# Performance work log

Measured on AMD Instinct MI355X. Metric: run time of the kernel, lower is better.

The kernel has to match this reference:

```python
import jax, jax.numpy as jnp
import numpy as np

DIM = 768
NC = 8            # ncontext
SIGMA = 0.5       # mask_sigma
SCALE = DIM ** (-0.5)
B, N = 256, 205   # N = 1 (CLS) + 14*14 (patches) + NC (concept tokens)


def setup_inputs() -> dict:
    key = jax.random.key(0)
    k1, k2, k3, k4 = jax.random.split(key, 4)
    x = jax.random.normal(k1, (B, N, DIM), dtype=jnp.float32)
    s = DIM ** (-0.5)
    Wq = jax.random.normal(k2, (DIM, DIM), dtype=jnp.float32) * s
    Wk = jax.random.normal(k3, (DIM, DIM), dtype=jnp.float32) * s
    Wv = jax.random.normal(k4, (DIM, DIM), dtype=jnp.float32) * s
    return {"x": x, "Wq": Wq, "Wk": Wk, "Wv": Wv}


def mask_attention_map(region):
    # region: [B, NC, HW] raw attention scores over the patch grid
    Bc, C, HW = region.shape
    H = W = int(np.sqrt(HW))  # 14
    amap = region.reshape(Bc, C, H, W)
    loc = jnp.argmax(amap.reshape(Bc, C, -1), axis=2)  # flat argmax (non-differentiable)
    max_y = (loc // H).astype(jnp.float32)[:, :, None, None]  # row of max
    max_x = (loc % H).astype(jnp.float32)[:, :, None, None]   # col of max
    # Faithful to torch.meshgrid(x, y) 'ij' + reshape(H, W): xx varies along rows,
    # yy varies along cols, and xx is compared to max_x (col), yy to max_y (row).
    rows = jnp.arange(H, dtype=jnp.float32).reshape(1, 1, H, 1)  # xx
    cols = jnp.arange(W, dtype=jnp.float32).reshape(1, 1, 1, W)  # yy
    g = jnp.exp(-((rows - max_x) ** 2 + (cols - max_y) ** 2) / (2.0 * SIGMA ** 2))
    g = g / jnp.max(g.reshape(Bc, C, -1), axis=2)[:, :, None, None]
    return (amap * g).reshape(Bc, C, HW)


def reference(x, Wq, Wk, Wv):
    # nn.Linear(dim, dim, bias=False): y = x @ W.T
    q = jnp.einsum('bnd,ed->bne', x, Wq)
    k = jnp.einsum('bnd,ed->bne', x, Wk)
    v = jnp.einsum('bnd,ed->bne', x, Wv)
    attn = jnp.einsum('bqd,bkd->bqk', q, k)  # [B, N, N] raw scores
    # gaussian-mask the concept-token -> patch region (pre-softmax, in-place write-back)
    region = mask_attention_map(attn[:, -NC:, 1:-NC])
    attn = attn.at[:, -NC:, 1:-NC].set(region)
    attn = jax.nn.softmax(attn * SCALE, axis=-1)
    out = jnp.einsum('bqk,bkd->bqd', attn, v)
    return attn[:, None], out
```

## Files before the change

### kernel.cpp

```cpp
#include <hip/hip_runtime.h>
#include <hip/hip_bf16.h>

#define NB   256
#define NT   205
#define DIMD 768
#define NCC  8
#define NPP  196
#define LDY  1536
#define SCL  0.03608439182435161f

using u16 = unsigned short;
using u32 = unsigned int;
using bf16x8 = __attribute__((ext_vector_type(8))) short;
using f32x4  = __attribute__((ext_vector_type(4))) float;

#define WS_WB   0ul
#define WS_YV   3538944ul
#define WS_PB   164757504ul
#define DO_OUT  43033600ul
#define DO_XB   43033600ul
#define DO_M    143696896ul
#define DO_Z    149988352ul
#define DO_REGM 157885440ul

__device__ __forceinline__ u16 f2bf(float f) {
  u32 u = __float_as_uint(f);
  u += 0x7FFFu + ((u >> 16) & 1u);
  return (u16)(u >> 16);
}

__device__ __forceinline__ void gld16(const void* g, void* l) {
  __builtin_amdgcn_global_load_lds((const __attribute__((address_space(1))) u32*)g,
                                   (__attribute__((address_space(3))) u32*)l, 16, 0, 0);
}

__device__ __forceinline__ f32x4 mfma16(bf16x8 a, bf16x8 b, f32x4 c) {
  return __builtin_amdgcn_mfma_f32_16x16x32_bf16(a, b, c, 0, 0, 0);
}

#define NGX 5038080
#define NGW 73728
__global__ __launch_bounds__(256) void k_cast2(const float* __restrict__ x, u16* __restrict__ xb,
                                               const float* __restrict__ wv, u16* __restrict__ wbv) {
  int i = blockIdx.x * 256 + threadIdx.x;
  const float* s; u16* d; size_t g;
  if (i < NGX) { s = x; d = xb; g = (size_t)i; }
  else if (i < NGX + NGW) { s = wv; d = wbv; g = (size_t)(i - NGX); }
  else return;
  const float4* s4 = (const float4*)s;
  float4 a = s4[2*g], b = s4[2*g + 1];
  union { u16 h[8]; uint4 v; } r;
  r.h[0]=f2bf(a.x); r.h[1]=f2bf(a.y); r.h[2]=f2bf(a.z); r.h[3]=f2bf(a.w);
  r.h[4]=f2bf(b.x); r.h[5]=f2bf(b.y); r.h[6]=f2bf(b.z); r.h[7]=f2bf(b.w);
  *(uint4*)(d + 8*g) = r.v;
}

__global__ __launch_bounds__(256) void k_yv(const u16* __restrict__ A, const u16* __restrict__ Bt, u16* __restrict__ C) {
  __shared__ u16 As[128*32];
  __shared__ u16 Bs[128*32];
  const int tid = threadIdx.x, wid = tid >> 6, lane = tid & 63;
  const int swz = (blockIdx.x & 7) * 615 + (blockIdx.x >> 3);
  const int bm = swz / 12, bn = swz % 12;
  const size_t m0 = (size_t)bm * 128;
  const int n0 = bn * 128;
  const int wr = (wid >> 1) * 64, wc = (wid & 1) * 64;
  const int fr = lane & 15, fg = lane >> 4;
  const int eb0 = (wid*2+0)*512, eb1 = (wid*2+1)*512;
  const int e0 = eb0 + lane*8, e1 = eb1 + lane*8;
  const int r0 = e0 >> 5, c0 = e0 & 31, r1 = e1 >> 5, c1 = e1 & 31;
  f32x4 acc[4][4] = {};
  for (int k0 = 0; k0 < 768; k0 += 32) {
    gld16(A + (m0 + r0)*768 + k0 + c0, (char*)As + 2*eb0);
    gld16(A + (m0 + r1)*768 + k0 + c1, (char*)As + 2*eb1);
    gld16(Bt + (size_t)(n0 + r0)*768 + k0 + c0, (char*)Bs + 2*eb0);
    gld16(Bt + (size_t)(n0 + r1)*768 + k0 + c1, (char*)Bs + 2*eb1);
    __syncthreads();
    bf16x8 av[4], bv[4];
    #pragma unroll
    for (int m = 0; m < 4; ++m) av[m] = *(const bf16x8*)&As[(wr + m*16 + fr)*32 + fg*8];
    #pragma unroll
    for (int n = 0; n < 4; ++n) bv[n] = *(const bf16x8*)&Bs[(wc + n*16 + fr)*32 + fg*8];
    #pragma unroll
    for (int m = 0; m < 4; ++m)
      #pragma unroll
      for (int n = 0; n < 4; ++n)
        acc[m][n] = mfma16(av[m], bv[n], acc[m][n]);
    __syncthreads();
  }
  #pragma unroll
  for (int m = 0; m < 4; ++m) {
    #pragma unroll
    for (int j = 0; j < 4; ++j) {
      size_t row = m0 + wr + m*16 + fg*4 + j;
      u16* cp = C + row*LDY + n0 + wc;
      #pragma unroll
      for (int n = 0; n < 4; ++n) cp[n*16 + fr] = f2bf(acc[m][n][j]);
    }
  }
}

template<int AM, bool BT, bool CB>
__global__ __launch_bounds__(256) void k_gemm32(const float* __restrict__ A, const float* __restrict__ Bm,
                                                float* __restrict__ C, u16* __restrict__ Cb,
                                                int lda, int ldb, int ldc, int K, int nbn) {
  __shared__ float As[16][68];
  __shared__ float Bs[16][68];
  const int tid = threadIdx.x;
  const int m0 = (blockIdx.x / nbn) * 64, n0 = (blockIdx.x % nbn) * 64;
  const int ty = tid >> 4, tx = tid & 15;
  const int sr = tid >> 2, sk = (tid & 3) * 4;
  float acc[4][4] = {};
  for (int k0 = 0; k0 < K; k0 += 16) {
    if (AM == 1) {
      const int ak = tid >> 4, am = (tid & 15) * 4;
      float4 av = *(const float4*)&A[(size_t)(k0 + ak) * lda + m0 + am];
      *(float4*)&As[ak][am] = av;
    } else {
      size_t arow = (size_t)(m0 + sr);
      if (AM == 2) arow = (arow >> 3) * 205 + 197 + (arow & 7);
      float4 av = *(const float4*)&A[arow * lda + k0 + sk];
      As[sk+0][sr] = av.x; As[sk+1][sr] = av.y; As[sk+2][sr] = av.z; As[sk+3][sr] = av.w;
    }
    if (BT) {
      float4 bv = *(const float4*)&Bm[(size_t)(n0 + sr) * ldb + k0 + sk];
      Bs[sk+0][sr] = bv.x; Bs[sk+1][sr] = bv.y; Bs[sk+2][sr] = bv.z; Bs[sk+3][sr] = bv.w;
    } else {
      const int bk = tid >> 4, bn4 = (tid & 15) * 4;
      float4 bv = *(const float4*)&Bm[(size_t)(k0 + bk) * ldb + n0 + bn4];
      *(float4*)&Bs[bk][bn4] = bv;
    }
    __syncthreads();
    #pragma unroll
    for (int kk = 0; kk < 16; ++kk) {
      float4 a4 = *(const float4*)&As[kk][ty*4];
      float4 b4 = *(const float4*)&Bs[kk][tx*4];
      float a[4] = {a4.x, a4.y, a4.z, a4.w};
      float b[4] = {b4.x, b4.y, b4.z, b4.w};
      #pragma unroll
      for (int i = 0; i < 4; ++i)
        #pragma unroll
        for (int j = 0; j < 4; ++j) acc[i][j] += a[i]*b[j];
    }
    __syncthreads();
  }
  #pragma unroll
  for (int i = 0; i < 4; ++i) {
    float4 o = {acc[i][0], acc[i][1], acc[i][2], acc[i][3]};
    *(float4*)&C[(size_t)(m0 + ty*4 + i) * ldc + n0 + tx*4] = o;
    if (CB) {
      union { u16 h[4]; uint2 v; } w;
      w.h[0] = f2bf(o.x); w.h[1] = f2bf(o.y); w.h[2] = f2bf(o.z); w.h[3] = f2bf(o.w);
      *(uint2*)&Cb[(size_t)(m0 + ty*4 + i) * ldc + n0 + tx*4] = w.v;
    }
  }
}

__global__ __launch_bounds__(256) void k_regmask(const float* __restrict__ zz, const float* __restrict__ x,
                                                 float* __restrict__ regm) {
  const int b = blockIdx.x, tid = threadIdx.x;
  __shared__ float zs[8*768];
  __shared__ float rs[8*NPP];
  for (int idx = tid; idx < 8*768; idx += 256) zs[idx] = zz[(size_t)b*8*768 + idx];
  __syncthreads();
  if (tid < NPP) {
    const float* xp = x + ((size_t)b*NT + 1 + tid) * DIMD;
    float a0=0,a1=0,a2=0,a3=0,a4=0,a5=0,a6=0,a7=0;
    #pragma unroll 4
    for (int d = 0; d < 768; d += 4) {
      float4 xv = *(const float4*)&xp[d];
      a0 += zs[0*768+d]*xv.x + zs[0*768+d+1]*xv.y + zs[0*768+d+2]*xv.z + zs[0*768+d+3]*xv.w;
      a1 += zs[1*768+d]*xv.x + zs[1*768+d+1]*xv.y + zs[1*768+d+2]*xv.z + zs[1*768+d+3]*xv.w;
      a2 += zs[2*768+d]*xv.x + zs[2*768+d+1]*xv.y + zs[2*768+d+2]*xv.z + zs[2*768+d+3]*xv.w;
      a3 += zs[3*768+d]*xv.x + zs[3*768+d+1]*xv.y + zs[3*768+d+2]*xv.z + zs[3*768+d+3]*xv.w;
      a4 += zs[4*768+d]*xv.x + zs[4*768+d+1]*xv.y + zs[4*768+d+2]*xv.z + zs[4*768+d+3]*xv.w;
      a5 += zs[5*768+d]*xv.x + zs[5*768+d+1]*xv.y + zs[5*768+d+2]*xv.z + zs[5*768+d+3]*xv.w;
      a6 += zs[6*768+d]*xv.x + zs[6*768+d+1]*xv.y + zs[6*768+d+2]*xv.z + zs[6*768+d+3]*xv.w;
      a7 += zs[7*768+d]*xv.x + zs[7*768+d+1]*xv.y + zs[7*768+d+2]*xv.z + zs[7*768+d+3]*xv.w;
    }
    rs[0*NPP+tid]=a0; rs[1*NPP+tid]=a1; rs[2*NPP+tid]=a2; rs[3*NPP+tid]=a3;
    rs[4*NPP+tid]=a4; rs[5*NPP+tid]=a5; rs[6*NPP+tid]=a6; rs[7*NPP+tid]=a7;
  }
  __syncthreads();
  const int w = tid >> 6, lane = tid & 63;
  #pragma unroll
  for (int cc = 0; cc < 2; ++cc) {
    const int c = 2*w + cc;
    float best = -1e30f; int bi = 0;
    #pragma unroll
    for (int q = 0; q < 4; ++q) {
      int p = lane + q*64;
      if (p < NPP) {
        float v = rs[c*NPP + p];
        if (v > best) { best = v; bi = p; }
      }
    }
    for (int off = 32; off; off >>= 1) {
      float ov = __shfl_xor(best, off);
      int   oi = __shfl_xor(bi, off);
      if (ov > best || (ov == best && oi < bi)) { best = ov; bi = oi; }
    }
    const float mx = (float)(bi % 14), my = (float)(bi / 14);
    #pragma unroll
    for (int q = 0; q < 4; ++q) {
      int p = lane + q*64;
      if (p < NPP) {
        float hh = (float)(p / 14), ww = (float)(p % 14);
        float d2 = (hh - mx)*(hh - mx) + (ww - my)*(ww - my);
        regm[((size_t)b*NCC + c)*NPP + p] = rs[c*NPP + p] * __expf(-2.0f * d2);
      }
    }
  }
}

__global__ __launch_bounds__(512) void k_sms(const u16* __restrict__ yv, const u16* __restrict__ xb,
                                             const float* __restrict__ regm, float* __restrict__ S,
                                             u16* __restrict__ pb) {
  __shared__ u16 Ys[128*40];
  __shared__ u16 Xs[208*40];
  const int tid = threadIdx.x, wid = tid >> 6, lane = tid & 63;
  const int sw = (blockIdx.x & 7) * 64 + (blockIdx.x >> 3);
  const int b = sw >> 1, it = sw & 1;
  const int i0 = it * 128;
  const int fr = lane & 15, fg = lane >> 4;
  const int sr2 = tid >> 2, sc2 = (tid & 3) * 8;
  const size_t xbase = (size_t)b * NT;
  const u16* gy = yv + (xbase + (size_t)min(i0 + sr2, NT-1)) * LDY + sc2;
  const u16* gx = xb + xbase * DIMD;
  const int xr2 = min(sr2 + 128, NT-1);
  f32x4 acc[13] = {};
  for (int k0 = 0; k0 < 768; k0 += 32) {
    *(bf16x8*)&Ys[sr2*40 + sc2] = *(const bf16x8*)(gy + k0);
    *(bf16x8*)&Xs[sr2*40 + sc2] = *(const bf16x8*)&gx[(size_t)sr2*DIMD + k0 + sc2];
    if (sr2 < 80)
      *(bf16x8*)&Xs[(sr2 + 128)*40 + sc2] = *(const bf16x8*)&gx[(size_t)xr2*DIMD + k0 + sc2];
    __syncthreads();
    bf16x8 a = *(const bf16x8*)&Ys[(wid*16 + fr)*40 + fg*8];
    #pragma unroll
    for (int n = 0; n < 13; ++n) {
      bf16x8 bv = *(const bf16x8*)&Xs[(n*16 + fr)*40 + fg*8];
      acc[n] = mfma16(a, bv, acc[n]);
    }
    __syncthreads();
  }
  #pragma unroll
  for (int jj = 0; jj < 4; ++jj) {
    const int gi = i0 + wid*16 + fg*4 + jj;
    if (gi >= 197 && gi < NT) {
      const float* rm = regm + ((size_t)b*NCC + (gi - 197)) * NPP;
      #pragma unroll
      for (int n = 0; n < 13; ++n) {
        int c = n*16 + fr;
        if (c >= 1 && c <= NPP) acc[n][jj] = rm[c - 1];
      }
    }
    float m = -1e30f;
    #pragma unroll
    for (int n = 0; n < 13; ++n) {
      int c = n*16 + fr;
      float v = (c < NT) ? acc[n][jj] * SCL : -1e30f;
      acc[n][jj] = v;
      m = fmaxf(m, v);
    }
    m = fmaxf(m, __shfl_xor(m, 1)); m = fmaxf(m, __shfl_xor(m, 2));
    m = fmaxf(m, __shfl_xor(m, 4)); m = fmaxf(m, __shfl_xor(m, 8));
    float s = 0.f;
    #pragma unroll
    for (int n = 0; n < 13; ++n) {
      int c = n*16 + fr;
      float e = (c < NT) ? __expf(acc[n][jj] - m) : 0.f;
      acc[n][jj] = e;
      s += e;
    }
    s += __shfl_xor(s, 1); s += __shfl_xor(s, 2);
    s += __shfl_xor(s, 4); s += __shfl_xor(s, 8);
    const float inv = 1.0f / s;
    if (gi < NT) {
      float* So = S + ((size_t)b*NT + gi) * NT;
      u16*   pr = pb + ((size_t)b*NT + gi) * 256;
      #pragma unroll
      for (int n = 0; n < 13; ++n) {
        int c = n*16 + fr;
        if (c < NT) So[c] = acc[n][jj] * inv;
      }
      #pragma unroll
      for (int n = 0; n < 16; ++n) {
        int c = n*16 + fr;
        u16 v = 0;
        if (n < 13 && c < NT) v = f2bf(acc[n][jj] * inv);
        pr[c] = v;
      }
    }
  }
}

__global__ __launch_bounds__(256) void k_pv(const u16* __restrict__ pb, const u16* __restrict__ yv,
                                            float* __restrict__ out) {
  __shared__ u16 Ps[64*232];
  __shared__ u16 Vt_s[64*232];
  const int tid = threadIdx.x, wid = tid >> 6, lane = tid & 63;
  const int swz = (blockIdx.x & 7) * 1536 + (blockIdx.x >> 3);
  const int b = swz / 48, t = swz % 48;
  const int i0 = (t / 12) * 64, e0 = (t % 12) * 64;
  const int wr = (wid >> 1) * 32, wc = (wid & 1) * 32;
  const int fr = lane & 15, fg = lane >> 4;
  {
    const int sr = tid >> 2, cb = (tid & 3) * 8;
    const int ip = min(i0 + sr, NT-1);
    const u16* Pp = pb + ((size_t)b*NT + ip) * 256;
    #pragma unroll
    for (int j = 0; j < 7; ++j) {
      const int col = cb + 32*j;
      *(bf16x8*)&Ps[sr*232 + col] = *(const bf16x8*)&Pp[col];
    }
  }
  {
    const int vr = tid >> 3, g = tid & 7;
    const int vks = vr ^ ((g & 3) << 3);
    #pragma unroll
    for (int c = 0; c < 7; ++c) {
      const int kv = min(c*32 + vr, NT-1);
      bf16x8 vv = *(const bf16x8*)&yv[((size_t)b*NT + kv)*LDY + 768 + e0 + g*8];
      #pragma unroll
      for (int j = 0; j < 8; ++j) Vt_s[(g*8 + j)*232 + c*32 + vks] = (u16)vv[j];
    }
  }
  __syncthreads();
  const int er0 = wc + fr, er1 = wc + 16 + fr;
  const int kx0 = (fg*8) ^ (((er0 >> 3) & 3) << 3);
  const int kx1 = (fg*8) ^ (((er1 >> 3) & 3) << 3);
  f32x4 acc[2][2] = {};
  #pragma unroll
  for (int k = 0; k < 7; ++k) {
    bf16x8 av[2], bv[2];
    av[0] = *(const bf16x8*)&Ps[(wr      + fr)*232 + k*32 + fg*8];
    av[1] = *(const bf16x8*)&Ps[(wr + 16 + fr)*232 + k*32 + fg*8];
    bv[0] = *(const bf16x8*)&Vt_s[er0*232 + k*32 + kx0];
    bv[1] = *(const bf16x8*)&Vt_s[er1*232 + k*32 + kx1];
    acc[0][0] = mfma16(av[0], bv[0], acc[0][0]);
    acc[0][1] = mfma16(av[0], bv[1], acc[0][1]);
    acc[1][0] = mfma16(av[1], bv[0], acc[1][0]);
    acc[1][1] = mfma16(av[1], bv[1], acc[1][1]);
  }
  #pragma unroll
  for (int m = 0; m < 2; ++m)
    #pragma unroll
    for (int n = 0; n < 2; ++n)
      #pragma unroll
      for (int j = 0; j < 4; ++j) {
        int i = i0 + wr + m*16 + fg*4 + j;
        int e = e0 + wc + n*16 + fr;
        if (i < NT)
          out[((size_t)b*NT + i)*DIMD + e] = acc[m][n][j];
      }
}

extern "C" void kernel_launch(void* const* d_in, const int* in_sizes, int n_in,
                              void* d_out, int out_size, void* d_ws, size_t ws_size,
                              hipStream_t stream) {
  const float* x  = (const float*)d_in[0];
  const float* Wq = (const float*)d_in[1];
  const float* Wk = (const float*)d_in[2];
  const float* Wv = (const float*)d_in[3];
  char* ws = (char*)d_ws;
  char* ob = (char*)d_out;

  u16*   wb   = (u16*)(ws + WS_WB);
  u16*   yv   = (u16*)(ws + WS_YV);
  u16*   pb   = (u16*)(ws + WS_PB);

  float* S    = (float*)ob;
  float* outp = (float*)(ob + DO_OUT);
  u16*   xb   = (u16*)(ob + DO_XB);
  float* Mt   = (float*)(ob + DO_M);
  float* zz   = (float*)(ob + DO_Z);
  float* regm = (float*)(ob + DO_REGM);

  k_cast2<<<19968, 256, 0, stream>>>(x, xb, Wv, wb + 589824);
  k_gemm32<1, false, true><<<144, 256, 0, stream>>>(Wk, Wq, Mt, wb, 768, 768, 768, 768, 12);
  k_yv<<<4920, 256, 0, stream>>>(xb, wb, yv);
  k_gemm32<2, true, false><<<384, 256, 0, stream>>>(x, Mt, zz, nullptr, 768, 768, 768, 768, 12);
  k_regmask<<<256, 256, 0, stream>>>(zz, x, regm);
  k_sms<<<512, 512, 0, stream>>>(yv, xb, regm, S, pb);
  k_pv<<<12288, 256, 0, stream>>>(pb, yv, outp);
}
```

Baseline: 525.9 us.

## Merge independent cast/GEMM launches into two heterogeneous block-dispatched kernels

Combines the cast kernel with the Wk·Wq fp32 GEMM into one launch, and the zz fp32 GEMM with the bf16 MFMA yv GEMM into a second launch, dispatching by block index. This removes two kernel launches and lets the small, low-occupancy fp32 GEMMs overlap with the large cast and yv work instead of running serially. Risks include higher register/LDS footprint per block from the union of code paths, which can lower occupancy for the dominant yv blocks, and the small GEMM blocks becoming a tail if scheduled late.

```diff
diff --git a/kernel.cpp b/kernel.cpp
--- a/kernel.cpp
+++ b/kernel.cpp
@@ -38,28 +38,77 @@
   return __builtin_amdgcn_mfma_f32_16x16x32_bf16(a, b, c, 0, 0, 0);
 }
 
-#define NGX 5038080
-#define NGW 73728
-__global__ __launch_bounds__(256) void k_cast2(const float* __restrict__ x, u16* __restrict__ xb,
-                                               const float* __restrict__ wv, u16* __restrict__ wbv) {
-  int i = blockIdx.x * 256 + threadIdx.x;
-  const float* s; u16* d; size_t g;
-  if (i < NGX) { s = x; d = xb; g = (size_t)i; }
-  else if (i < NGX + NGW) { s = wv; d = wbv; g = (size_t)(i - NGX); }
-  else return;
+__device__ __forceinline__ void dev_cast(const float* __restrict__ s, u16* __restrict__ d, int i, int n8) {
+  if (i >= n8) return;
   const float4* s4 = (const float4*)s;
-  float4 a = s4[2*g], b = s4[2*g + 1];
+  float4 a = s4[2*(size_t)i], b = s4[2*(size_t)i + 1];
   union { u16 h[8]; uint4 v; } r;
   r.h[0]=f2bf(a.x); r.h[1]=f2bf(a.y); r.h[2]=f2bf(a.z); r.h[3]=f2bf(a.w);
   r.h[4]=f2bf(b.x); r.h[5]=f2bf(b.y); r.h[6]=f2bf(b.z); r.h[7]=f2bf(b.w);
-  *(uint4*)(d + 8*g) = r.v;
-}
-
-__global__ __launch_bounds__(256) void k_yv(const u16* __restrict__ A, const u16* __restrict__ Bt, u16* __restrict__ C) {
+  *(uint4*)(d + 8*(size_t)i) = r.v;
+}
+
+template<int AM, bool BT, bool CB>
+__device__ void dev_gemm32(const float* __restrict__ A, const float* __restrict__ Bm,
+                           float* __restrict__ C, u16* __restrict__ Cb,
+                           int lda, int ldb, int ldc, int K, int nbn, int bid) {
+  __shared__ float As[16][68];
+  __shared__ float Bs[16][68];
+  const int tid = threadIdx.x;
+  const int m0 = (bid / nbn) * 64, n0 = (bid % nbn) * 64;
+  const int ty = tid >> 4, tx = tid & 15;
+  const int sr = tid >> 2, sk = (tid & 3) * 4;
+  float acc[4][4] = {};
+  for (int k0 = 0; k0 < K; k0 += 16) {
+    if (AM == 1) {
+      const int ak = tid >> 4, am = (tid & 15) * 4;
+      float4 av = *(const float4*)&A[(size_t)(k0 + ak) * lda + m0 + am];
+      *(float4*)&As[ak][am] = av;
+    } else {
+      size_t arow = (size_t)(m0 + sr);
+      if (AM == 2) arow = (arow >> 3) * 205 + 197 + (arow & 7);
+      float4 av = *(const float4*)&A[arow * lda + k0 + sk];
+      As[sk+0][sr] = av.x; As[sk+1][sr] = av.y; As[sk+2][sr] = av.z; As[sk+3][sr] = av.w;
+    }
+    if (BT) {
+      float4 bv = *(const float4*)&Bm[(size_t)(n0 + sr) * ldb + k0 + sk];
+      Bs[sk+0][sr] = bv.x; Bs[sk+1][sr] = bv.y; Bs[sk+2][sr] = bv.z; Bs[sk+3][sr] = bv.w;
+    } else {
+      const int bk = tid >> 4, bn4 = (tid & 15) * 4;
+      float4 bv = *(const float4*)&Bm[(size_t)(k0 + bk) * ldb + n0 + bn4];
+      *(float4*)&Bs[bk][bn4] = bv;
+    }
+    __syncthreads();
+    #pragma unroll
+    for (int kk = 0; kk < 16; ++kk) {
+      float4 a4 = *(const float4*)&As[kk][ty*4];
+      float4 b4 = *(const float4*)&Bs[kk][tx*4];
+      float a[4] = {a4.x, a4.y, a4.z, a4.w};
+      float b[4] = {b4.x, b4.y, b4.z, b4.w};
+      #pragma unroll
+      for (int i = 0; i < 4; ++i)
+        #pragma unroll
+        for (int j = 0; j < 4; ++j) acc[i][j] += a[i]*b[j];
+    }
+    __syncthreads();
+  }
+  #pragma unroll
+  for (int i = 0; i < 4; ++i) {
+    float4 o = {acc[i][0], acc[i][1], acc[i][2], acc[i][3]};
+    *(float4*)&C[(size_t)(m0 + ty*4 + i) * ldc + n0 + tx*4] = o;
+    if (CB) {
+      union { u16 h[4]; uint2 v; } w;
+      w.h[0] = f2bf(o.x); w.h[1] = f2bf(o.y); w.h[2] = f2bf(o.z); w.h[3] = f2bf(o.w);
+      *(uint2*)&Cb[(size_t)(m0 + ty*4 + i) * ldc + n0 + tx*4] = w.v;
+    }
+  }
+}
+
+__device__ void dev_yv(const u16* __restrict__ A, const u16* __restrict__ Bt, u16* __restrict__ C, int bid) {
   __shared__ u16 As[128*32];
   __shared__ u16 Bs[128*32];
   const int tid = threadIdx.x, wid = tid >> 6, lane = tid & 63;
-  const int swz = (blockIdx.x & 7) * 615 + (blockIdx.x >> 3);
+  const int swz = (bid & 7) * 615 + (bid >> 3);
   const int bm = swz / 12, bn = swz % 12;
   const size_t m0 = (size_t)bm * 128;
   const int n0 = bn * 128;
@@ -99,59 +148,31 @@
   }
 }
 
-template<int AM, bool BT, bool CB>
-__global__ __launch_bounds__(256) void k_gemm32(const float* __restrict__ A, const float* __restrict__ Bm,
-                                                float* __restrict__ C, u16* __restrict__ Cb,
-                                                int lda, int ldb, int ldc, int K, int nbn) {
-  __shared__ float As[16][68];
-  __shared__ float Bs[16][68];
-  const int tid = threadIdx.x;
-  const int m0 = (blockIdx.x / nbn) * 64, n0 = (blockIdx.x % nbn) * 64;
-  const int ty = tid >> 4, tx = tid & 15;
-  const int sr = tid >> 2, sk = (tid & 3) * 4;
-  float acc[4][4] = {};
-  for (int k0 = 0; k0 < K; k0 += 16) {
-    if (AM == 1) {
-      const int ak = tid >> 4, am = (tid & 15) * 4;
-      float4 av = *(const float4*)&A[(size_t)(k0 + ak) * lda + m0 + am];
-      *(float4*)&As[ak][am] = av;
-    } else {
-      size_t arow = (size_t)(m0 + sr);
-      if (AM == 2) arow = (arow >> 3) * 205 + 197 + (arow & 7);
-      float4 av = *(const float4*)&A[arow * lda + k0 + sk];
-      As[sk+0][sr] = av.x; As[sk+1][sr] = av.y; As[sk+2][sr] = av.z; As[sk+3][sr] = av.w;
-    }
-    if (BT) {
-      float4 bv = *(const float4*)&Bm[(size_t)(n0 + sr) * ldb + k0 + sk];
-      Bs[sk+0][sr] = bv.x; Bs[sk+1][sr] = bv.y; Bs[sk+2][sr] = bv.z; Bs[sk+3][sr] = bv.w;
-    } else {
-      const int bk = tid >> 4, bn4 = (tid & 15) * 4;
-      float4 bv = *(const float4*)&Bm[(size_t)(k0 + bk) * ldb + n0 + bn4];
-      *(float4*)&Bs[bk][bn4] = bv;
-    }
-    __syncthreads();
-    #pragma unroll
-    for (int kk = 0; kk < 16; ++kk) {
-      float4 a4 = *(const float4*)&As[kk][ty*4];
-      float4 b4 = *(const float4*)&Bs[kk][tx*4];
-      float a[4] = {a4.x, a4.y, a4.z, a4.w};
-      float b[4] = {b4.x, b4.y, b4.z, b4.w};
-      #pragma unroll
-      for (int i = 0; i < 4; ++i)
-        #pragma unroll
-        for (int j = 0; j < 4; ++j) acc[i][j] += a[i]*b[j];
-    }
-    __syncthreads();
-  }
-  #pragma unroll
-  for (int i = 0; i < 4; ++i) {
-    float4 o = {acc[i][0], acc[i][1], acc[i][2], acc[i][3]};
-    *(float4*)&C[(size_t)(m0 + ty*4 + i) * ldc + n0 + tx*4] = o;
-    if (CB) {
-      union { u16 h[4]; uint2 v; } w;
-      w.h[0] = f2bf(o.x); w.h[1] = f2bf(o.y); w.h[2] = f2bf(o.z); w.h[3] = f2bf(o.w);
-      *(uint2*)&Cb[(size_t)(m0 + ty*4 + i) * ldc + n0 + tx*4] = w.v;
-    }
+#define NGX 5038080
+#define NGW 73728
+__global__ __launch_bounds__(256) void k_L1(const float* __restrict__ Wk, const float* __restrict__ Wq,
+                                            float* __restrict__ Mt, u16* __restrict__ wb,
+                                            const float* __restrict__ x, u16* __restrict__ xb,
+                                            const float* __restrict__ wv, u16* __restrict__ wbv) {
+  const int bid = blockIdx.x;
+  if (bid < 144) {
+    dev_gemm32<1, false, true>(Wk, Wq, Mt, wb, 768, 768, 768, 768, 12, bid);
+  } else {
+    int i = (bid - 144) * 256 + threadIdx.x;
+    if (i < NGX) dev_cast(x, xb, i, NGX);
+    else dev_cast(wv, wbv, i - NGX, NGW);
+  }
+}
+
+__global__ __launch_bounds__(256) void k_L2(const float* __restrict__ x, const float* __restrict__ Mt,
+                                            float* __restrict__ zz,
+                                            const u16* __restrict__ xb, const u16* __restrict__ wb,
+                                            u16* __restrict__ yv) {
+  const int bid = blockIdx.x;
+  if (bid < 384) {
+    dev_gemm32<2, true, false>(x, Mt, zz, nullptr, 768, 768, 768, 768, 12, bid);
+  } else {
+    dev_yv(xb, wb, yv, bid - 384);
   }
 }
 
@@ -375,10 +396,8 @@
   float* zz   = (float*)(ob + DO_Z);
   float* regm = (float*)(ob + DO_REGM);
 
-  k_cast2<<<19968, 256, 0, stream>>>(x, xb, Wv, wb + 589824);
-  k_gemm32<1, false, true><<<144, 256, 0, stream>>>(Wk, Wq, Mt, wb, 768, 768, 768, 768, 12);
-  k_yv<<<4920, 256, 0, stream>>>(xb, wb, yv);
-  k_gemm32<2, true, false><<<384, 256, 0, stream>>>(x, Mt, zz, nullptr, 768, 768, 768, 768, 12);
+  k_L1<<<20112, 256, 0, stream>>>(Wk, Wq, Mt, wb, x, xb, Wv, wb + 589824);
+  k_L2<<<5304, 256, 0, stream>>>(x, Mt, zz, xb, wb, yv);
   k_regmask<<<256, 256, 0, stream>>>(zz, x, regm);
   k_sms<<<512, 512, 0, stream>>>(yv, xb, regm, S, pb);
   k_pv<<<12288, 256, 0, stream>>>(pb, yv, outp);
```

Measured after the change: 497.7 us. 5.4% less time.
